# Optimization experiments

Hardware: AMD Instinct MI355X
Metric: run time of the kernel (lower is better)

## Reference

```python
import jax, jax.numpy as jnp
import numpy as np

WINDOW_SIZE = 16
DILATION = 2

B, L, H, E = 2, 4096, 8, 64


def setup_inputs() -> dict:
    key = jax.random.key(0)
    kq, kk, kv = jax.random.split(key, 3)
    queries = jax.random.normal(kq, (B, L, H, E), dtype=jnp.float32)
    keys = jax.random.normal(kk, (B, L, H, E), dtype=jnp.float32)
    values = jax.random.normal(kv, (B, L, H, E), dtype=jnp.float32)
    return {"queries": queries, "keys": keys, "values": values}


def _window_indices(Lk: int):
    # offsets: [-r, ..., r] * dilation ; idx[l, w] = clamp(l + off[w], 0, Lk-1)
    offsets = jnp.arange(-WINDOW_SIZE, WINDOW_SIZE + 1) * DILATION
    idx = jnp.arange(Lk)[:, None] + offsets[None, :]
    return jnp.clip(idx, 0, Lk - 1)


def reference(queries, keys, values):
    # queries/keys/values: [B, L, H, E]
    Bq, Lq, Hq, Eq = queries.shape
    scale = 1.0 / jnp.sqrt(jnp.asarray(Eq, queries.dtype))
    idx = _window_indices(keys.shape[1])
    K_win = keys[:, idx]
    V_win = values[:, idx]
    scores = jnp.einsum('blhe,blwhe->blhw', queries, K_win) * scale
    A = jax.nn.softmax(scores, axis=-1)
    V = jnp.einsum('blhw,blwhe->blhe', A, V_win)    # [B, L, H, E]
    return V
```

## Files before the change

### kernel.cpp

```cpp
#include <hip/hip_runtime.h>
#include <hip/hip_bf16.h>
#include <math.h>

#define B_    2
#define L_    4096
#define H_    8
#define E_    64
#define VTSTR 136
#define PSTR  72

using frag8 = __attribute__((ext_vector_type(8))) short;
using fl4   = __attribute__((ext_vector_type(4))) float;

__device__ __forceinline__ unsigned short f2bf(float f) {
    return __builtin_bit_cast(unsigned short, __float2bfloat16(f));
}
__device__ __forceinline__ frag8 pack8(float4 a, float4 b) {
    frag8 r;
    r[0] = (short)f2bf(a.x); r[1] = (short)f2bf(a.y);
    r[2] = (short)f2bf(a.z); r[3] = (short)f2bf(a.w);
    r[4] = (short)f2bf(b.x); r[5] = (short)f2bf(b.y);
    r[6] = (short)f2bf(b.z); r[7] = (short)f2bf(b.w);
    return r;
}

__global__ __launch_bounds__(256, 4)
void lda_kernel(const float* __restrict__ Q, const float* __restrict__ K,
                const float* __restrict__ V, float* __restrict__ O) {
    __shared__ unsigned short Vt[E_ * VTSTR];
    __shared__ unsigned short Pw[4 * 16 * PSTR];

    const int tid  = threadIdx.x;
    const int lane = tid & 63;
    const int wave = tid >> 6;
    const int col  = lane & 15;
    const int quad = lane >> 4;
    const int p    = wave & 1;
    const int t    = wave >> 1;
    const int l0   = blockIdx.x * 64;
    const int bh   = blockIdx.y;
    const int b    = bh >> 3;
    const int h    = bh & 7;

    const size_t base = ((size_t)(b * L_) * H_ + h) * E_;
    const int    rs   = H_ * E_;

    #pragma unroll
    for (int i = 0; i < 8; ++i) {
        int g   = wave * 8 + i;
        int pg  = g >> 4;
        int rh0 = (g & 15) * 4;
        float a0, a1, a2, a3;
        {
            int rg = l0 - 32 + 2 * (rh0 + 0) + pg; rg = rg < 0 ? 0 : (rg > L_-1 ? L_-1 : rg);
            a0 = V[base + (size_t)rg * rs + lane];
        }
        {
            int rg = l0 - 32 + 2 * (rh0 + 1) + pg; rg = rg < 0 ? 0 : (rg > L_-1 ? L_-1 : rg);
            a1 = V[base + (size_t)rg * rs + lane];
        }
        {
            int rg = l0 - 32 + 2 * (rh0 + 2) + pg; rg = rg < 0 ? 0 : (rg > L_-1 ? L_-1 : rg);
            a2 = V[base + (size_t)rg * rs + lane];
        }
        {
            int rg = l0 - 32 + 2 * (rh0 + 3) + pg; rg = rg < 0 ? 0 : (rg > L_-1 ? L_-1 : rg);
            a3 = V[base + (size_t)rg * rs + lane];
        }
        uint2 u;
        u.x = (unsigned)f2bf(a0) | ((unsigned)f2bf(a1) << 16);
        u.y = (unsigned)f2bf(a2) | ((unsigned)f2bf(a3) << 16);
        *(uint2*)&Vt[lane * VTSTR + pg * 64 + rh0] = u;
    }

    const int lq = l0 + 2 * (16 * t + col) + p;
    frag8 aq[2];
    #pragma unroll
    for (int k = 0; k < 2; ++k) {
        const float* qp = Q + base + (size_t)lq * rs + k * 32 + quad * 8;
        aq[k] = pack8(*(const float4*)qp, *(const float4*)(qp + 4));
    }

    fl4 S[3];
    #pragma unroll
    for (int c = 0; c < 3; ++c) {
        int rhat = 16 * (t + c) + col;
        int rg = l0 - 32 + 2 * rhat + p;
        rg = rg < 0 ? 0 : (rg > L_ - 1 ? L_ - 1 : rg);
        const float* kp = K + base + (size_t)rg * rs;
        fl4 acc = {0.f, 0.f, 0.f, 0.f};
        #pragma unroll
        for (int k = 0; k < 2; ++k) {
            frag8 bk = pack8(*(const float4*)(kp + k * 32 + quad * 8),
                             *(const float4*)(kp + k * 32 + quad * 8 + 4));
            acc = __builtin_amdgcn_mfma_f32_16x16x32_bf16(aq[k], bk, acc, 0, 0, 0);
        }
        S[c] = acc;
    }

    float pw[3][4];
    #pragma unroll
    for (int c = 0; c < 3; ++c)
        #pragma unroll
        for (int reg = 0; reg < 4; ++reg)
            pw[c][reg] = exp2f(S[c][reg] * 0.18033688011112043f);

    const int pb = wave * 16 * PSTR;
    #pragma unroll
    for (int i = 0; i < 3; ++i) {
        int idx = lane + 64 * i;
        if (idx < 144) { uint4 z = {0u,0u,0u,0u}; *(uint4*)&Pw[pb + idx * 8] = z; }
    }
    #pragma unroll
    for (int reg = 0; reg < 4; ++reg) {
        int off = quad * 4 + reg;
        #pragma unroll
        for (int c = 0; c < 3; ++c) {
            int j = 16 * c + col - off;
            if (j >= 0 && j <= 32)
                Pw[pb + off * PSTR + 16 * (t + c) + col] = f2bf(pw[c][reg]);
        }
    }

    frag8 ap[2];
    #pragma unroll
    for (int k = 0; k < 2; ++k)
        ap[k] = *(const frag8*)&Pw[pb + col * PSTR + k * 32 + quad * 8];

    frag8 ones;
    #pragma unroll
    for (int i = 0; i < 8; ++i) ones[i] = (short)0x3F80;
    fl4 sums = {0.f, 0.f, 0.f, 0.f};
    sums = __builtin_amdgcn_mfma_f32_16x16x32_bf16(ap[0], ones, sums, 0, 0, 0);
    sums = __builtin_amdgcn_mfma_f32_16x16x32_bf16(ap[1], ones, sums, 0, 0, 0);
    float inv[4];
    #pragma unroll
    for (int reg = 0; reg < 4; ++reg) inv[reg] = __builtin_amdgcn_rcpf(sums[reg]);

    __syncthreads();

    #pragma unroll
    for (int nt = 0; nt < 4; ++nt) {
        fl4 c = {0.f, 0.f, 0.f, 0.f};
        #pragma unroll
        for (int k = 0; k < 2; ++k) {
            frag8 bv = *(const frag8*)&Vt[(nt * 16 + col) * VTSTR + p * 64 + k * 32 + quad * 8];
            c = __builtin_amdgcn_mfma_f32_16x16x32_bf16(ap[k], bv, c, 0, 0, 0);
        }
        #pragma unroll
        for (int reg = 0; reg < 4; ++reg) {
            int l = 2 * (16 * t + quad * 4 + reg) + p;
            O[base + (size_t)(l0 + l) * rs + nt * 16 + col] = c[reg] * inv[reg];
        }
    }
}

extern "C" void kernel_launch(void* const* d_in, const int* in_sizes, int n_in,
                              void* d_out, int out_size, void* d_ws, size_t ws_size,
                              hipStream_t stream) {
    const float* Q = (const float*)d_in[0];
    const float* K = (const float*)d_in[1];
    const float* V = (const float*)d_in[2];
    float* O = (float*)d_out;

    dim3 grid(L_ / 64, B_ * H_);
    dim3 block(256);
    lda_kernel<<<grid, block, 0, stream>>>(Q, K, V, O);
}
```

Measured before the change: 96.32 us.

## Swizzle blocks across XCDs, defer V staging, and use nontemporal output stores

Switches to a 1D grid and remaps block IDs so each XCD gets a contiguous range of sequence tiles across all batch-heads. The aim is to improve L2 reuse of the overlapping K/V halo rows. V loads are now issued into registers after the QK MFMAs and written to LDS only just before the barrier, so their latency can overlap with the score and softmax work. Output stores become nontemporal to avoid polluting cache, at the cost of 32 extra VGPRs for the buffered V values, which may lower occupancy.

```diff
diff --git a/kernel.cpp b/kernel.cpp
--- a/kernel.cpp
+++ b/kernel.cpp
@@ -37,41 +37,18 @@
     const int quad = lane >> 4;
     const int p    = wave & 1;
     const int t    = wave >> 1;
-    const int l0   = blockIdx.x * 64;
-    const int bh   = blockIdx.y;
-    const int b    = bh >> 3;
-    const int h    = bh & 7;
+
+    const int g   = blockIdx.x;
+    const int xcd = g & 7;
+    const int s   = g >> 3;
+    const int bh  = s & 15;
+    const int xt  = (xcd << 3) | (s >> 4);
+    const int l0  = xt * 64;
+    const int b   = bh >> 3;
+    const int h   = bh & 7;
 
     const size_t base = ((size_t)(b * L_) * H_ + h) * E_;
     const int    rs   = H_ * E_;
-
-    #pragma unroll
-    for (int i = 0; i < 8; ++i) {
-        int g   = wave * 8 + i;
-        int pg  = g >> 4;
-        int rh0 = (g & 15) * 4;
-        float a0, a1, a2, a3;
-        {
-            int rg = l0 - 32 + 2 * (rh0 + 0) + pg; rg = rg < 0 ? 0 : (rg > L_-1 ? L_-1 : rg);
-            a0 = V[base + (size_t)rg * rs + lane];
-        }
-        {
-            int rg = l0 - 32 + 2 * (rh0 + 1) + pg; rg = rg < 0 ? 0 : (rg > L_-1 ? L_-1 : rg);
-            a1 = V[base + (size_t)rg * rs + lane];
-        }
-        {
-            int rg = l0 - 32 + 2 * (rh0 + 2) + pg; rg = rg < 0 ? 0 : (rg > L_-1 ? L_-1 : rg);
-            a2 = V[base + (size_t)rg * rs + lane];
-        }
-        {
-            int rg = l0 - 32 + 2 * (rh0 + 3) + pg; rg = rg < 0 ? 0 : (rg > L_-1 ? L_-1 : rg);
-            a3 = V[base + (size_t)rg * rs + lane];
-        }
-        uint2 u;
-        u.x = (unsigned)f2bf(a0) | ((unsigned)f2bf(a1) << 16);
-        u.y = (unsigned)f2bf(a2) | ((unsigned)f2bf(a3) << 16);
-        *(uint2*)&Vt[lane * VTSTR + pg * 64 + rh0] = u;
-    }
 
     const int lq = l0 + 2 * (16 * t + col) + p;
     frag8 aq[2];
@@ -96,6 +73,20 @@
             acc = __builtin_amdgcn_mfma_f32_16x16x32_bf16(aq[k], bk, acc, 0, 0, 0);
         }
         S[c] = acc;
+    }
+
+    float va[32];
+    #pragma unroll
+    for (int i = 0; i < 8; ++i) {
+        int gi  = wave * 8 + i;
+        int pg  = gi >> 4;
+        int rh0 = (gi & 15) * 4;
+        #pragma unroll
+        for (int j = 0; j < 4; ++j) {
+            int rg = l0 - 32 + 2 * (rh0 + j) + pg;
+            rg = rg < 0 ? 0 : (rg > L_ - 1 ? L_ - 1 : rg);
+            va[i * 4 + j] = V[base + (size_t)rg * rs + lane];
+        }
     }
 
     float pw[3][4];
@@ -137,6 +128,16 @@
     #pragma unroll
     for (int reg = 0; reg < 4; ++reg) inv[reg] = __builtin_amdgcn_rcpf(sums[reg]);
 
+    #pragma unroll
+    for (int i = 0; i < 8; ++i) {
+        int gi  = wave * 8 + i;
+        int pg  = gi >> 4;
+        int rh0 = (gi & 15) * 4;
+        uint2 u;
+        u.x = (unsigned)f2bf(va[i*4+0]) | ((unsigned)f2bf(va[i*4+1]) << 16);
+        u.y = (unsigned)f2bf(va[i*4+2]) | ((unsigned)f2bf(va[i*4+3]) << 16);
+        *(uint2*)&Vt[lane * VTSTR + pg * 64 + rh0] = u;
+    }
     __syncthreads();
 
     #pragma unroll
@@ -150,7 +151,8 @@
         #pragma unroll
         for (int reg = 0; reg < 4; ++reg) {
             int l = 2 * (16 * t + quad * 4 + reg) + p;
-            O[base + (size_t)(l0 + l) * rs + nt * 16 + col] = c[reg] * inv[reg];
+            __builtin_nontemporal_store(c[reg] * inv[reg],
+                O + base + (size_t)(l0 + l) * rs + nt * 16 + col);
         }
     }
 }
@@ -163,7 +165,7 @@
     const float* V = (const float*)d_in[2];
     float* O = (float*)d_out;
 
-    dim3 grid(L_ / 64, B_ * H_);
+    dim3 grid(L_ / 64 * B_ * H_);
     dim3 block(256);
     lda_kernel<<<grid, block, 0, stream>>>(Q, K, V, O);
 }
```

Measured after the change: 91.80 us (median of 2 runs). 1.05x faster.
